# Performance work log

Hardware: AMD Instinct MI355X
Metric: run time of the kernel (lower is better)

## Reference

```python
import jax, jax.numpy as jnp
import numpy as np

B, L, D, K = 32, 4096, 1024, 64


def setup_inputs() -> dict:
    key = jax.random.key(0)
    k1, k2, k3, k4, k5 = jax.random.split(key, 5)
    feats = jax.random.normal(k1, (B, L, D), dtype=jnp.float32)
    assign_w = jax.random.normal(k2, (K, D), dtype=jnp.float32) * (1.0 / np.sqrt(D))
    assign_b = jax.random.normal(k3, (K,), dtype=jnp.float32) * 0.01
    centroids = jax.random.uniform(k4, (K, D), dtype=jnp.float32)
    # ensure at least one valid token per batch row (softmax over L stays finite)
    lens = jax.random.randint(k5, (B,), L // 2, L + 1, dtype=jnp.int32)
    return {"feats": feats, "lens": lens, "assign_w": assign_w,
            "assign_b": assign_b, "centroids": centroids}


def reference(feats, lens, assign_w, assign_b, centroids):
    # feats: (B,L,D); lens: (B,) int; assign_w: (K,D); assign_b: (K,); centroids: (K,D)
    Bq, Lq, Dq = feats.shape
    # padding mask; torch code slices to max(lens) first, but masked positions
    # contribute zero weight after softmax, so keeping full L is equivalent.
    mask = jnp.arange(Lq)[None, :] < lens[:, None]            # (B,L)
    logits = jnp.einsum('bld,kd->blk', feats, assign_w) + assign_b  # (B,L,K)
    logits = jnp.where(mask[:, :, None], logits, -jnp.inf)
    a = jax.nn.softmax(logits, axis=1)                         # softmax over L
    # (a[:,:,:,None] * (feats[:,:,None,:] - centroids)).sum(1) without
    # materializing the (B,L,K,D) residual tensor:
    s = a.sum(axis=1)                                          # (B,K), == 1 analytically
    vlad = jnp.einsum('blk,bld->bkd', a, feats) - s[..., None] * centroids[None]  # (B,K,D)
    out = vlad.min(axis=1)                                     # min over clusters -> (B,D)
    norm = jnp.maximum(jnp.linalg.norm(out, axis=-1, keepdims=True), 1e-12)
    return out / norm
```

## Files before the change

### kernel.cpp

```cpp
#include <hip/hip_runtime.h>
#include <math.h>

#define NB 32
#define NL 4096
#define ND 1024
#define NK 64
#define DTILE 128
#define S_SPLIT 4

typedef __bf16 bf16_t;
typedef __bf16 bf16x8 __attribute__((ext_vector_type(8)));
typedef __bf16 bf16x4 __attribute__((ext_vector_type(4)));
typedef float f32x4_t __attribute__((ext_vector_type(4)));

__global__ __launch_bounds__(256) void k_convw(const float* __restrict__ W,
                                               bf16_t* __restrict__ Wb) {
    const int i = (blockIdx.x * 256 + threadIdx.x) * 4;
    const float4 v = *(const float4*)(W + i);
    bf16x4 o;
    o[0] = (bf16_t)v.x; o[1] = (bf16_t)v.y; o[2] = (bf16_t)v.z; o[3] = (bf16_t)v.w;
    *(bf16x4*)(Wb + i) = o;
}

__global__ __launch_bounds__(256) void k_logits(const float* __restrict__ feats,
                                                const bf16_t* __restrict__ Wb,
                                                const float* __restrict__ bias,
                                                const int* __restrict__ lens,
                                                float* __restrict__ logitsT,
                                                float* __restrict__ pmax,
                                                float* __restrict__ psum) {
    const int bid = blockIdx.x;
    const int b = bid >> 6;
    const int chunk = bid & 63;
    const int l0 = chunk << 6;
    const int len = lens[b];
    if (l0 >= len) return;
    const int t = threadIdx.x;
    const int w = t >> 6;
    const int lane = t & 63;
    const int lr = lane & 15;
    const int oct = lane >> 4;
    const float* fp = feats + ((size_t)b * NL + l0 + w * 16 + lr) * ND + oct * 8;

    f32x4_t acc[4];
#pragma unroll
    for (int j = 0; j < 4; ++j) acc[j] = (f32x4_t){0.f, 0.f, 0.f, 0.f};

#pragma unroll 4
    for (int kk = 0; kk < 32; ++kk) {
        const int d = kk * 32;
        const float4 a0 = *(const float4*)(fp + d);
        const float4 a1 = *(const float4*)(fp + d + 4);
        bf16x8 af;
        af[0] = (bf16_t)a0.x; af[1] = (bf16_t)a0.y; af[2] = (bf16_t)a0.z; af[3] = (bf16_t)a0.w;
        af[4] = (bf16_t)a1.x; af[5] = (bf16_t)a1.y; af[6] = (bf16_t)a1.z; af[7] = (bf16_t)a1.w;
#pragma unroll
        for (int j = 0; j < 4; ++j) {
            const bf16x8 bf = *(const bf16x8*)(Wb + (size_t)(j * 16 + lr) * ND + d + oct * 8);
            acc[j] = __builtin_amdgcn_mfma_f32_16x16x32_bf16(af, bf, acc[j], 0, 0, 0);
        }
    }
    float vals[4][4];
#pragma unroll
    for (int j = 0; j < 4; ++j) {
        const int k = j * 16 + lr;
        const float bs = bias[k];
#pragma unroll
        for (int r = 0; r < 4; ++r) vals[j][r] = acc[j][r] + bs;
        const int lb = l0 + w * 16 + oct * 4;
        float4 st = make_float4(vals[j][0], vals[j][1], vals[j][2], vals[j][3]);
        *(float4*)(logitsT + ((size_t)b * NK + k) * NL + lb) = st;
    }
    __shared__ float red[64][17];
    __shared__ float bm[64];
    const int slot = w * 4 + oct;
    const int lbase = l0 + w * 16 + oct * 4;
#pragma unroll
    for (int j = 0; j < 4; ++j) {
        float vm = -1e30f;
#pragma unroll
        for (int r = 0; r < 4; ++r)
            if (lbase + r < len) vm = fmaxf(vm, vals[j][r]);
        red[j * 16 + lr][slot] = vm;
    }
    __syncthreads();
    if (t < 64) {
        float m = -1e30f;
#pragma unroll
        for (int q = 0; q < 16; ++q) m = fmaxf(m, red[t][q]);
        bm[t] = m;
    }
    __syncthreads();
#pragma unroll
    for (int j = 0; j < 4; ++j) {
        const float mk = bm[j * 16 + lr];
        float sj = 0.f;
#pragma unroll
        for (int r = 0; r < 4; ++r)
            if (lbase + r < len) sj += __expf(vals[j][r] - mk);
        red[j * 16 + lr][slot] = sj;
    }
    __syncthreads();
    if (t < 64) {
        float ssum = 0.f;
#pragma unroll
        for (int q = 0; q < 16; ++q) ssum += red[t][q];
        pmax[((size_t)b * 64 + chunk) * 64 + t] = bm[t];
        psum[((size_t)b * 64 + chunk) * 64 + t] = ssum;
    }
}

__global__ void k_sm2(const float* __restrict__ pmax, const float* __restrict__ psum,
                      const int* __restrict__ lens,
                      float* __restrict__ mbuf2) {
    const int b = blockIdx.x;
    const int k = threadIdx.x;
    const int nc = (lens[b] + 63) >> 6;
    float m = -1e30f;
    for (int c = 0; c < nc; ++c) m = fmaxf(m, pmax[((size_t)b * 64 + c) * 64 + k]);
    float s = 0.f;
    for (int c = 0; c < nc; ++c)
        s += psum[((size_t)b * 64 + c) * 64 + k] * __expf(pmax[((size_t)b * 64 + c) * 64 + k] - m);
    mbuf2[b * 64 + k] = m + logf(s);
}

__global__ __launch_bounds__(256, 4) void k_aggregate(const float* __restrict__ feats,
                                                      const float* __restrict__ logitsT,
                                                      const int* __restrict__ lens,
                                                      const float* __restrict__ mbuf2,
                                                      float* __restrict__ pO) {
    const int bid = blockIdx.x;
    const int s  = bid & 3;
    const int dc = (bid >> 2) & 7;
    const int b  = bid >> 5;
    const int d0 = dc * DTILE;
    const int t = threadIdx.x;
    const int w = t >> 6;
    const int lane = t & 63;
    const int lr = lane & 15;
    const int oct = lane >> 4;
    const int len = lens[b];
    const int nT = (len + 63) >> 6;
    const int t0 = (nT * s) >> 2;
    const int t1 = (nT * (s + 1)) >> 2;

    __shared__ char ldsb[32 * 1024];
    char* const fH = ldsb;
    char* const fL = ldsb + 16 * 1024;

    const int kk = w * 16 + lr;
    const float ms2k = mbuf2[b * 64 + kk];
    const float* lgrow = logitsT + ((size_t)b * NK + kk) * NL;

    const int c4 = (t & 31) * 4;
    const int lf0 = (t >> 5) * 4;

    f32x4_t acc[8];
#pragma unroll
    for (int n = 0; n < 8; ++n) acc[n] = (f32x4_t){0.f, 0.f, 0.f, 0.f};

    float4 plg[4];
    float4 pf[2][4];

#define LOADT(tile_)                                                                     \
    {                                                                                    \
        const int lb_ = (tile_) * 64;                                                    \
        plg[0] = *(const float4*)(lgrow + lb_ + oct * 8);                                \
        plg[1] = *(const float4*)(lgrow + lb_ + oct * 8 + 4);                            \
        plg[2] = *(const float4*)(lgrow + lb_ + 32 + oct * 8);                           \
        plg[3] = *(const float4*)(lgrow + lb_ + 32 + oct * 8 + 4);                       \
        _Pragma("unroll")                                                                \
        for (int p_ = 0; p_ < 2; ++p_) {                                                 \
            _Pragma("unroll")                                                            \
            for (int i_ = 0; i_ < 4; ++i_)                                               \
                pf[p_][i_] = *(const float4*)(feats +                                    \
                    ((size_t)b * NL + lb_ + p_ * 32 + lf0 + i_) * ND + d0 + c4);         \
        }                                                                                \
    }

    if (t0 < t1) LOADT(t0);

    for (int tile = t0; tile < t1; ++tile) {
        const int l0 = tile * 64;
        bf16x8 afH[2], afL[2];
#pragma unroll
        for (int ks = 0; ks < 2; ++ks) {
#pragma unroll
            for (int h = 0; h < 2; ++h) {
                const float4 v = plg[ks * 2 + h];
                const int lbase = l0 + ks * 32 + oct * 8 + h * 4;
                float av[4];
                av[0] = (lbase + 0 < len) ? __expf(v.x - ms2k) : 0.f;
                av[1] = (lbase + 1 < len) ? __expf(v.y - ms2k) : 0.f;
                av[2] = (lbase + 2 < len) ? __expf(v.z - ms2k) : 0.f;
                av[3] = (lbase + 3 < len) ? __expf(v.w - ms2k) : 0.f;
#pragma unroll
                for (int c = 0; c < 4; ++c) {
                    const bf16_t hi = (bf16_t)av[c];
                    afH[ks][h * 4 + c] = hi;
                    afL[ks][h * 4 + c] = (bf16_t)(av[c] - (float)hi);
                }
            }
        }
        __syncthreads();
#pragma unroll
        for (int p = 0; p < 2; ++p) {
            const int l4 = p * 32 + lf0;
#pragma unroll
            for (int j = 0; j < 4; ++j) {
                const int d = c4 + j;
                bf16x4 hi, lo;
                const float e0 = (&pf[p][0].x)[j];
                const float e1 = (&pf[p][1].x)[j];
                const float e2 = (&pf[p][2].x)[j];
                const float e3 = (&pf[p][3].x)[j];
                hi[0] = (bf16_t)e0; hi[1] = (bf16_t)e1; hi[2] = (bf16_t)e2; hi[3] = (bf16_t)e3;
                lo[0] = (bf16_t)(e0 - (float)hi[0]); lo[1] = (bf16_t)(e1 - (float)hi[1]);
                lo[2] = (bf16_t)(e2 - (float)hi[2]); lo[3] = (bf16_t)(e3 - (float)hi[3]);
                const int chunk = (l4 >> 3) ^ ((d ^ (d >> 3)) & 7);
                const int off = d * 128 + (chunk << 4) + (l4 & 7) * 2;
                *(bf16x4*)(fH + off) = hi;
                *(bf16x4*)(fL + off) = lo;
            }
        }
        if (tile + 1 < t1) LOADT(tile + 1);
        __syncthreads();
#pragma unroll
        for (int ks = 0; ks < 2; ++ks) {
            const int cbase = ks * 4 + oct;
#pragma unroll
            for (int n = 0; n < 8; ++n) {
                const int d = n * 16 + lr;
                const int foff = d * 128 + ((cbase ^ ((d ^ (d >> 3)) & 7)) << 4);
                const bf16x8 bfH = *(const bf16x8*)(fH + foff);
                const bf16x8 bfL = *(const bf16x8*)(fL + foff);
                acc[n] = __builtin_amdgcn_mfma_f32_16x16x32_bf16(afH[ks], bfH, acc[n], 0, 0, 0);
                acc[n] = __builtin_amdgcn_mfma_f32_16x16x32_bf16(afH[ks], bfL, acc[n], 0, 0, 0);
                acc[n] = __builtin_amdgcn_mfma_f32_16x16x32_bf16(afL[ks], bfH, acc[n], 0, 0, 0);
            }
        }
    }
#undef LOADT
    float* po = pO + ((size_t)((b * 8 + dc) * S_SPLIT + s)) * (NK * DTILE);
#pragma unroll
    for (int n = 0; n < 8; ++n) {
#pragma unroll
        for (int r = 0; r < 4; ++r) {
            const int k = w * 16 + oct * 4 + r;
            po[k * DTILE + n * 16 + lr] = acc[n][r];
        }
    }
}

__global__ __launch_bounds__(128) void k_combine(const float* __restrict__ pO,
                                                 const float* __restrict__ centroids,
                                                 float* __restrict__ outun) {
    const int b = blockIdx.x >> 3;
    const int d = (blockIdx.x & 7) * 128 + threadIdx.x;
    const int dc = d >> 7;
    const int dl = d & 127;
    const float* base = pO + ((size_t)(b * 8 + dc)) * S_SPLIT * NK * DTILE;
    float mn = 1e30f;
    for (int k = 0; k < NK; ++k) {
        float v = 0.f;
#pragma unroll
        for (int s = 0; s < S_SPLIT; ++s) v += base[(size_t)(s * NK + k) * DTILE + dl];
        v -= centroids[(size_t)k * ND + d];
        mn = fminf(mn, v);
    }
    outun[(size_t)b * ND + d] = mn;
}

__global__ __launch_bounds__(256) void k_norm(const float* __restrict__ outun,
                                              float* __restrict__ out) {
    const int b = blockIdx.x;
    const int t = threadIdx.x;
    float ss = 0.f;
    for (int d = t; d < ND; d += 256) {
        const float v = outun[(size_t)b * ND + d];
        ss += v * v;
    }
#pragma unroll
    for (int off = 32; off > 0; off >>= 1) ss += __shfl_down(ss, off);
    __shared__ float red[4];
    if ((t & 63) == 0) red[t >> 6] = ss;
    __syncthreads();
    const float tot = red[0] + red[1] + red[2] + red[3];
    const float inv = 1.0f / fmaxf(sqrtf(tot), 1e-12f);
    for (int d = t; d < ND; d += 256) out[(size_t)b * ND + d] = outun[(size_t)b * ND + d] * inv;
}

extern "C" void kernel_launch(void* const* d_in, const int* in_sizes, int n_in,
                              void* d_out, int out_size, void* d_ws, size_t ws_size,
                              hipStream_t stream) {
    const float* feats     = (const float*)d_in[0];
    const int*   lens      = (const int*)d_in[1];
    const float* W         = (const float*)d_in[2];
    const float* bias      = (const float*)d_in[3];
    const float* centroids = (const float*)d_in[4];
    float* out = (float*)d_out;

    char* ws = (char*)d_ws;
    size_t off = 0;
    bf16_t* Wb     = (bf16_t*)(ws + off); off += (size_t)NK * ND * sizeof(bf16_t);
    float* logitsT = (float*)(ws + off);  off += (size_t)NB * NL * NK * sizeof(float);
    float* pmax    = (float*)(ws + off);  off += (size_t)NB * 64 * NK * sizeof(float);
    float* psum    = (float*)(ws + off);  off += (size_t)NB * 64 * NK * sizeof(float);
    float* mbuf2   = (float*)(ws + off);  off += (size_t)NB * NK * sizeof(float);
    float* outun   = (float*)(ws + off);  off += (size_t)NB * ND * sizeof(float);
    float* pO      = (float*)(ws + off);

    k_convw<<<NK * ND / 1024, 256, 0, stream>>>(W, Wb);
    k_logits<<<NB * (NL / 64), 256, 0, stream>>>(feats, Wb, bias, lens, logitsT, pmax, psum);
    k_sm2<<<NB, 64, 0, stream>>>(pmax, psum, lens, mbuf2);
    k_aggregate<<<NB * 8 * S_SPLIT, 256, 0, stream>>>(feats, logitsT, lens, mbuf2, pO);
    k_combine<<<NB * 8, 128, 0, stream>>>(pO, centroids, outun);
    k_norm<<<NB, 256, 0, stream>>>(outun, out);
}
```

Before: 351.8 us.

## Double logits rows per block and drop feats low-part split in aggregation

The logits kernel now gives each block 128 sequence positions instead of 64. Each wave computes two 16-row MFMA tiles that share the same weight fragment loads, which halves the per-block weight traffic and the block count. The aggregation kernel stops storing and multiplying the bf16 low part of feats. It drops one of the three MFMAs per step and halves the LDS footprint, at the cost of accuracy in the feats operand, which is now plain bf16.

Measured after the change: 284.6 us. 1.24x faster.

```diff
diff --git a/kernel.cpp b/kernel.cpp
--- a/kernel.cpp
+++ b/kernel.cpp
@@ -30,9 +30,9 @@
                                                 float* __restrict__ pmax,
                                                 float* __restrict__ psum) {
     const int bid = blockIdx.x;
-    const int b = bid >> 6;
-    const int chunk = bid & 63;
-    const int l0 = chunk << 6;
+    const int b = bid >> 5;
+    const int chunk = bid & 31;
+    const int l0 = chunk << 7;
     const int len = lens[b];
     if (l0 >= len) return;
     const int t = threadIdx.x;
@@ -40,73 +40,90 @@
     const int lane = t & 63;
     const int lr = lane & 15;
     const int oct = lane >> 4;
-    const float* fp = feats + ((size_t)b * NL + l0 + w * 16 + lr) * ND + oct * 8;
-
-    f32x4_t acc[4];
-#pragma unroll
-    for (int j = 0; j < 4; ++j) acc[j] = (f32x4_t){0.f, 0.f, 0.f, 0.f};
-
-#pragma unroll 4
+    const float* fp0 = feats + ((size_t)b * NL + l0 + w * 32 + lr) * ND + oct * 8;
+    const float* fp1 = fp0 + (size_t)16 * ND;
+
+    f32x4_t acc[2][4];
+#pragma unroll
+    for (int m = 0; m < 2; ++m)
+#pragma unroll
+        for (int j = 0; j < 4; ++j) acc[m][j] = (f32x4_t){0.f, 0.f, 0.f, 0.f};
+
+#pragma unroll 2
     for (int kk = 0; kk < 32; ++kk) {
         const int d = kk * 32;
-        const float4 a0 = *(const float4*)(fp + d);
-        const float4 a1 = *(const float4*)(fp + d + 4);
-        bf16x8 af;
-        af[0] = (bf16_t)a0.x; af[1] = (bf16_t)a0.y; af[2] = (bf16_t)a0.z; af[3] = (bf16_t)a0.w;
-        af[4] = (bf16_t)a1.x; af[5] = (bf16_t)a1.y; af[6] = (bf16_t)a1.z; af[7] = (bf16_t)a1.w;
+        const float4 a0 = *(const float4*)(fp0 + d);
+        const float4 a1 = *(const float4*)(fp0 + d + 4);
+        const float4 a2 = *(const float4*)(fp1 + d);
+        const float4 a3 = *(const float4*)(fp1 + d + 4);
+        bf16x8 af0, af1;
+        af0[0] = (bf16_t)a0.x; af0[1] = (bf16_t)a0.y; af0[2] = (bf16_t)a0.z; af0[3] = (bf16_t)a0.w;
+        af0[4] = (bf16_t)a1.x; af0[5] = (bf16_t)a1.y; af0[6] = (bf16_t)a1.z; af0[7] = (bf16_t)a1.w;
+        af1[0] = (bf16_t)a2.x; af1[1] = (bf16_t)a2.y; af1[2] = (bf16_t)a2.z; af1[3] = (bf16_t)a2.w;
+        af1[4] = (bf16_t)a3.x; af1[5] = (bf16_t)a3.y; af1[6] = (bf16_t)a3.z; af1[7] = (bf16_t)a3.w;
 #pragma unroll
         for (int j = 0; j < 4; ++j) {
             const bf16x8 bf = *(const bf16x8*)(Wb + (size_t)(j * 16 + lr) * ND + d + oct * 8);
-            acc[j] = __builtin_amdgcn_mfma_f32_16x16x32_bf16(af, bf, acc[j], 0, 0, 0);
-        }
-    }
-    float vals[4][4];
-#pragma unroll
-    for (int j = 0; j < 4; ++j) {
-        const int k = j * 16 + lr;
-        const float bs = bias[k];
-#pragma unroll
-        for (int r = 0; r < 4; ++r) vals[j][r] = acc[j][r] + bs;
-        const int lb = l0 + w * 16 + oct * 4;
-        float4 st = make_float4(vals[j][0], vals[j][1], vals[j][2], vals[j][3]);
-        *(float4*)(logitsT + ((size_t)b * NK + k) * NL + lb) = st;
-    }
-    __shared__ float red[64][17];
+            acc[0][j] = __builtin_amdgcn_mfma_f32_16x16x32_bf16(af0, bf, acc[0][j], 0, 0, 0);
+            acc[1][j] = __builtin_amdgcn_mfma_f32_16x16x32_bf16(af1, bf, acc[1][j], 0, 0, 0);
+        }
+    }
+    float vals[2][4][4];
+#pragma unroll
+    for (int m = 0; m < 2; ++m)
+#pragma unroll
+        for (int j = 0; j < 4; ++j) {
+            const int k = j * 16 + lr;
+            const float bs = bias[k];
+#pragma unroll
+            for (int r = 0; r < 4; ++r) vals[m][j][r] = acc[m][j][r] + bs;
+            const int lb = l0 + w * 32 + m * 16 + oct * 4;
+            float4 st = make_float4(vals[m][j][0], vals[m][j][1], vals[m][j][2], vals[m][j][3]);
+            *(float4*)(logitsT + ((size_t)b * NK + k) * NL + lb) = st;
+        }
+    __shared__ float red[64][33];
     __shared__ float bm[64];
-    const int slot = w * 4 + oct;
-    const int lbase = l0 + w * 16 + oct * 4;
-#pragma unroll
-    for (int j = 0; j < 4; ++j) {
-        float vm = -1e30f;
-#pragma unroll
-        for (int r = 0; r < 4; ++r)
-            if (lbase + r < len) vm = fmaxf(vm, vals[j][r]);
-        red[j * 16 + lr][slot] = vm;
+    const int slot = w * 8 + oct * 2;
+#pragma unroll
+    for (int m = 0; m < 2; ++m) {
+        const int lbase = l0 + w * 32 + m * 16 + oct * 4;
+#pragma unroll
+        for (int j = 0; j < 4; ++j) {
+            float vm = -1e30f;
+#pragma unroll
+            for (int r = 0; r < 4; ++r)
+                if (lbase + r < len) vm = fmaxf(vm, vals[m][j][r]);
+            red[j * 16 + lr][slot + m] = vm;
+        }
     }
     __syncthreads();
     if (t < 64) {
         float m = -1e30f;
 #pragma unroll
-        for (int q = 0; q < 16; ++q) m = fmaxf(m, red[t][q]);
+        for (int q = 0; q < 32; ++q) m = fmaxf(m, red[t][q]);
         bm[t] = m;
     }
     __syncthreads();
 #pragma unroll
-    for (int j = 0; j < 4; ++j) {
-        const float mk = bm[j * 16 + lr];
-        float sj = 0.f;
-#pragma unroll
-        for (int r = 0; r < 4; ++r)
-            if (lbase + r < len) sj += __expf(vals[j][r] - mk);
-        red[j * 16 + lr][slot] = sj;
+    for (int m = 0; m < 2; ++m) {
+        const int lbase = l0 + w * 32 + m * 16 + oct * 4;
+#pragma unroll
+        for (int j = 0; j < 4; ++j) {
+            const float mk = bm[j * 16 + lr];
+            float sj = 0.f;
+#pragma unroll
+            for (int r = 0; r < 4; ++r)
+                if (lbase + r < len) sj += __expf(vals[m][j][r] - mk);
+            red[j * 16 + lr][slot + m] = sj;
+        }
     }
     __syncthreads();
     if (t < 64) {
         float ssum = 0.f;
 #pragma unroll
-        for (int q = 0; q < 16; ++q) ssum += red[t][q];
-        pmax[((size_t)b * 64 + chunk) * 64 + t] = bm[t];
-        psum[((size_t)b * 64 + chunk) * 64 + t] = ssum;
+        for (int q = 0; q < 32; ++q) ssum += red[t][q];
+        pmax[((size_t)b * 32 + chunk) * 64 + t] = bm[t];
+        psum[((size_t)b * 32 + chunk) * 64 + t] = ssum;
     }
 }
 
@@ -115,12 +132,12 @@
                       float* __restrict__ mbuf2) {
     const int b = blockIdx.x;
     const int k = threadIdx.x;
-    const int nc = (lens[b] + 63) >> 6;
+    const int nc = (lens[b] + 127) >> 7;
     float m = -1e30f;
-    for (int c = 0; c < nc; ++c) m = fmaxf(m, pmax[((size_t)b * 64 + c) * 64 + k]);
+    for (int c = 0; c < nc; ++c) m = fmaxf(m, pmax[((size_t)b * 32 + c) * 64 + k]);
     float s = 0.f;
     for (int c = 0; c < nc; ++c)
-        s += psum[((size_t)b * 64 + c) * 64 + k] * __expf(pmax[((size_t)b * 64 + c) * 64 + k] - m);
+        s += psum[((size_t)b * 32 + c) * 64 + k] * __expf(pmax[((size_t)b * 32 + c) * 64 + k] - m);
     mbuf2[b * 64 + k] = m + logf(s);
 }
 
@@ -144,9 +161,7 @@
     const int t0 = (nT * s) >> 2;
     const int t1 = (nT * (s + 1)) >> 2;
 
-    __shared__ char ldsb[32 * 1024];
-    char* const fH = ldsb;
-    char* const fL = ldsb + 16 * 1024;
+    __shared__ char fH[16 * 1024];
 
     const int kk = w * 16 + lr;
     const float ms2k = mbuf2[b * 64 + kk];
@@ -209,18 +224,14 @@
 #pragma unroll
             for (int j = 0; j < 4; ++j) {
                 const int d = c4 + j;
-                bf16x4 hi, lo;
-                const float e0 = (&pf[p][0].x)[j];
-                const float e1 = (&pf[p][1].x)[j];
-                const float e2 = (&pf[p][2].x)[j];
-                const float e3 = (&pf[p][3].x)[j];
-                hi[0] = (bf16_t)e0; hi[1] = (bf16_t)e1; hi[2] = (bf16_t)e2; hi[3] = (bf16_t)e3;
-                lo[0] = (bf16_t)(e0 - (float)hi[0]); lo[1] = (bf16_t)(e1 - (float)hi[1]);
-                lo[2] = (bf16_t)(e2 - (float)hi[2]); lo[3] = (bf16_t)(e3 - (float)hi[3]);
+                bf16x4 hi;
+                hi[0] = (bf16_t)(&pf[p][0].x)[j];
+                hi[1] = (bf16_t)(&pf[p][1].x)[j];
+                hi[2] = (bf16_t)(&pf[p][2].x)[j];
+                hi[3] = (bf16_t)(&pf[p][3].x)[j];
                 const int chunk = (l4 >> 3) ^ ((d ^ (d >> 3)) & 7);
                 const int off = d * 128 + (chunk << 4) + (l4 & 7) * 2;
                 *(bf16x4*)(fH + off) = hi;
-                *(bf16x4*)(fL + off) = lo;
             }
         }
         if (tile + 1 < t1) LOADT(tile + 1);
@@ -233,9 +244,7 @@
                 const int d = n * 16 + lr;
                 const int foff = d * 128 + ((cbase ^ ((d ^ (d >> 3)) & 7)) << 4);
                 const bf16x8 bfH = *(const bf16x8*)(fH + foff);
-                const bf16x8 bfL = *(const bf16x8*)(fL + foff);
                 acc[n] = __builtin_amdgcn_mfma_f32_16x16x32_bf16(afH[ks], bfH, acc[n], 0, 0, 0);
-                acc[n] = __builtin_amdgcn_mfma_f32_16x16x32_bf16(afH[ks], bfL, acc[n], 0, 0, 0);
                 acc[n] = __builtin_amdgcn_mfma_f32_16x16x32_bf16(afL[ks], bfH, acc[n], 0, 0, 0);
             }
         }
@@ -304,14 +313,14 @@
     size_t off = 0;
     bf16_t* Wb     = (bf16_t*)(ws + off); off += (size_t)NK * ND * sizeof(bf16_t);
     float* logitsT = (float*)(ws + off);  off += (size_t)NB * NL * NK * sizeof(float);
-    float* pmax    = (float*)(ws + off);  off += (size_t)NB * 64 * NK * sizeof(float);
-    float* psum    = (float*)(ws + off);  off += (size_t)NB * 64 * NK * sizeof(float);
+    float* pmax    = (float*)(ws + off);  off += (size_t)NB * 32 * NK * sizeof(float);
+    float* psum    = (float*)(ws + off);  off += (size_t)NB * 32 * NK * sizeof(float);
     float* mbuf2   = (float*)(ws + off);  off += (size_t)NB * NK * sizeof(float);
     float* outun   = (float*)(ws + off);  off += (size_t)NB * ND * sizeof(float);
     float* pO      = (float*)(ws + off);
 
     k_convw<<<NK * ND / 1024, 256, 0, stream>>>(W, Wb);
-    k_logits<<<NB * (NL / 64), 256, 0, stream>>>(feats, Wb, bias, lens, logitsT, pmax, psum);
+    k_logits<<<NB * (NL / 128), 256, 0, stream>>>(feats, Wb, bias, lens, logitsT, pmax, psum);
     k_sm2<<<NB, 64, 0, stream>>>(pmax, psum, lens, mbuf2);
     k_aggregate<<<NB * 8 * S_SPLIT, 256, 0, stream>>>(feats, logitsT, lens, mbuf2, pO);
     k_combine<<<NB * 8, 128, 0, stream>>>(pO, centroids, outun);
```
